# Optimization experiments

Measured on AMD Instinct MI355X. Metric: run time of the kernel, lower is better.

Reference implementation:

```python
import jax, jax.numpy as jnp
import numpy as np

B, C, H, W, NP = 4, 512, 32, 32, 2048
NH = 4
EPS = 1e-5


def setup_inputs() -> dict:
    key = jax.random.key(0)
    ks = jax.random.split(key, 12)
    s = 0.02
    d = {}
    d["img_feature"] = jax.random.normal(ks[0], (B, C, H, W), jnp.float32)
    d["point_feature"] = jax.random.normal(ks[1], (B, C, NP), jnp.float32)
    d["mlp_w1"] = jax.random.normal(ks[2], (2 * C, C), jnp.float32) * s
    d["mlp_b1"] = jnp.zeros((2 * C,), jnp.float32)
    d["bn1_gamma"] = jnp.ones((2 * C,), jnp.float32)
    d["bn1_beta"] = jnp.zeros((2 * C,), jnp.float32)
    d["bn1_mean"] = jnp.zeros((2 * C,), jnp.float32)
    d["bn1_var"] = jnp.ones((2 * C,), jnp.float32)
    d["mlp_w2"] = jax.random.normal(ks[3], (C, 2 * C), jnp.float32) * s
    d["mlp_b2"] = jnp.zeros((C,), jnp.float32)
    d["bn2_gamma"] = jnp.ones((C,), jnp.float32)
    d["bn2_beta"] = jnp.zeros((C,), jnp.float32)
    d["bn2_mean"] = jnp.zeros((C,), jnp.float32)
    d["bn2_var"] = jnp.ones((C,), jnp.float32)
    d["attn_qw"] = jax.random.normal(ks[4], (3, C, C), jnp.float32) * s
    d["attn_qb"] = jnp.zeros((3, C), jnp.float32)
    d["attn_kw"] = jax.random.normal(ks[5], (3, C, C), jnp.float32) * s
    d["attn_kb"] = jnp.zeros((3, C), jnp.float32)
    d["attn_vw"] = jax.random.normal(ks[6], (3, C, C), jnp.float32) * s
    d["attn_vb"] = jnp.zeros((3, C), jnp.float32)
    d["attn_ln_g"] = jnp.ones((3, C), jnp.float32)
    d["attn_ln_b"] = jnp.zeros((3, C), jnp.float32)
    return d


def _bn(x, g, b, m, v):  # x: [B, C, N], eval-mode batchnorm over channel dim
    return (x - m[:, None]) * jax.lax.rsqrt(v[:, None] + EPS) * g[:, None] + b[:, None]


def _mlp(x, w1, b1, g1, be1, m1, v1, w2, b2, g2, be2, m2, v2):
    # 1x1 Conv1d == per-position linear over channels
    y = jnp.einsum('oc,bcn->bon', w1, x) + b1[:, None]
    y = jax.nn.relu(_bn(y, g1, be1, m1, v1))
    z = jnp.einsum('oc,bcn->bon', w2, y) + b2[:, None]
    return jax.nn.relu(_bn(z, g2, be2, m2, v2))


def _self_attn(x, qw, qb, kw, kb, vw, vb, lng, lnb):
    # x: [B, S, E]; NOTE: original scales by 1/sqrt(hidden_size), not head_dim
    Bq, S, E = x.shape
    Hd = E // NH
    q = (jnp.einsum('bse,de->bsd', x, qw) + qb).reshape(Bq, S, NH, Hd)
    k = (jnp.einsum('bse,de->bsd', x, kw) + kb).reshape(Bq, S, NH, Hd)
    v = (jnp.einsum('bse,de->bsd', x, vw) + vb).reshape(Bq, S, NH, Hd)
    scores = jnp.einsum('bqhd,bkhd->bhqk', q, k) * (float(E) ** -0.5)
    attn = jax.nn.softmax(scores, axis=-1)
    out = jnp.einsum('bhqk,bkhd->bqhd', attn, v).reshape(Bq, S, E)
    y = out + x
    mu = jnp.mean(y, axis=-1, keepdims=True)
    var = jnp.var(y, axis=-1, keepdims=True)
    return (y - mu) * jax.lax.rsqrt(var + EPS) * lng + lnb


def reference(img_feature, point_feature, mlp_w1, mlp_b1, bn1_gamma, bn1_beta,
              bn1_mean, bn1_var, mlp_w2, mlp_b2, bn2_gamma, bn2_beta, bn2_mean,
              bn2_var, attn_qw, attn_qb, attn_kw, attn_kb, attn_vw, attn_vb,
              attn_ln_g, attn_ln_b):
    b, c, h, w = img_feature.shape
    i_in = img_feature.reshape(b, c, h * w)  # [B, C, N_i]
    mlp_args = (mlp_w1, mlp_b1, bn1_gamma, bn1_beta, bn1_mean, bn1_var,
                mlp_w2, mlp_b2, bn2_gamma, bn2_beta, bn2_mean, bn2_var)
    p_feat = _mlp(point_feature, *mlp_args)  # [B, C, N_p]
    i_feat = _mlp(i_in, *mlp_args)           # [B, C, N_i]
    phi = jnp.einsum('bcp,bci->bpi', p_feat, i_feat) * (float(c) ** -0.5)
    phi_p = jax.nn.softmax(phi, axis=1)   # softmax over points
    phi_i = jax.nn.softmax(phi, axis=-1)  # softmax over image positions
    I_enh = jnp.einsum('bcp,bpi->bci', p_feat, phi_p)  # [B, C, N_i]
    P_enh = jnp.einsum('bci,bpi->bcp', i_feat, phi_i)  # [B, C, N_p]
    att = lambda x, j: _self_attn(x, attn_qw[j], attn_qb[j], attn_kw[j],
                                  attn_kb[j], attn_vw[j], attn_vb[j],
                                  attn_ln_g[j], attn_ln_b[j])
    I = att(jnp.swapaxes(I_enh, 1, 2), 0)  # [B, N_i, C]
    P = att(jnp.swapaxes(P_enh, 1, 2), 1)  # [B, N_p, C]
    joint = jnp.concatenate([P, I], axis=1)  # [B, N_p + N_i, C]
    return att(joint, 2)
```

## Files before the change

kernel.cpp:

```cpp
#include <hip/hip_runtime.h>
#include <math.h>

#define LN_EPS 1e-5f

typedef __attribute__((ext_vector_type(8))) short bf16x8;
typedef __attribute__((ext_vector_type(4))) float f32x4;

#define GLDS16(g, l) __builtin_amdgcn_global_load_lds( \
    (const __attribute__((address_space(1))) unsigned int*)(g), \
    (__attribute__((address_space(3))) unsigned int*)(l), 16, 0, 0)

__device__ __forceinline__ float b2f(unsigned short h) { return __uint_as_float(((unsigned)h) << 16); }
__device__ __forceinline__ unsigned short f2b(float f) {
  unsigned u = __float_as_uint(f);
  unsigned r = (u + 0x7fffu + ((u >> 16) & 1u)) >> 16;
  return (unsigned short)r;
}
__device__ __forceinline__ float ld(const float* p) { return *p; }
__device__ __forceinline__ float ld(const unsigned short* p) { return b2f(*p); }
__device__ __forceinline__ void st(float* p, float v) { *p = v; }
__device__ __forceinline__ void st(unsigned short* p, float v) { *p = f2b(v); }

__device__ __forceinline__ float bred_sum(float v, float* red) {
  for (int o = 32; o; o >>= 1) v += __shfl_down(v, o, 64);
  int wid = threadIdx.x >> 6;
  __syncthreads();
  if ((threadIdx.x & 63) == 0) red[wid] = v;
  __syncthreads();
  return red[0] + red[1] + red[2] + red[3];
}

__global__ void prep_all(
    const float* __restrict__ w1, const float* __restrict__ w2, const float* __restrict__ vw,
    const float* __restrict__ qw, const float* __restrict__ qb,
    const float* __restrict__ kw, const float* __restrict__ kb,
    const float* __restrict__ b1, const float* __restrict__ g1, const float* __restrict__ be1,
    const float* __restrict__ m1, const float* __restrict__ v1,
    const float* __restrict__ b2, const float* __restrict__ g2, const float* __restrict__ be2,
    const float* __restrict__ m2, const float* __restrict__ v2,
    unsigned short* __restrict__ w1b, unsigned short* __restrict__ w2b,
    unsigned short* __restrict__ vwb, unsigned short* __restrict__ qkw,
    float* __restrict__ qkbias, float* __restrict__ s1, float* __restrict__ f1,
    float* __restrict__ s2, float* __restrict__ f2)
{
  const float scl = 0.044194173824159216f * 1.4426950408889634f;
  int idx = blockIdx.x * 256 + threadIdx.x;
  {
    int j = idx >> 19; int r = idx & 524287; int n = r >> 9; int k = r & 511;
    float v = (n < 512) ? qw[j * 262144 + n * 512 + k] * scl
                        : kw[j * 262144 + (n - 512) * 512 + k];
    qkw[idx] = f2b(v);
  }
  if (idx < 524288) { w1b[idx] = f2b(w1[idx]); w2b[idx] = f2b(w2[idx]); }
  if (idx < 786432) vwb[idx] = f2b(vw[idx]);
  if (idx < 3072) {
    int j = idx >> 10, n = idx & 1023;
    qkbias[idx] = (n < 512) ? qb[j * 512 + n] * scl : kb[j * 512 + n - 512];
  }
  if (idx < 1024) { float s = g1[idx] * rsqrtf(v1[idx] + LN_EPS); s1[idx] = s; f1[idx] = (b1[idx] - m1[idx]) * s + be1[idx]; }
  if (idx < 512)  { float s = g2[idx] * rsqrtf(v2[idx] + LN_EPS); s2[idx] = s; f2[idx] = (b2[idx] - m2[idx]) * s + be2[idx]; }
}

template<typename TS, typename TD>
__global__ __launch_bounds__(256) void transpose_t(const TS* __restrict__ src,
    TD* __restrict__ dst, int R, int Cc, long sS, long sD) {
  __shared__ float t[32][33];
  src += (long)blockIdx.z * sS; dst += (long)blockIdx.z * sD;
  int c0 = blockIdx.x * 32, r0 = blockIdx.y * 32;
  int tx = threadIdx.x & 31, ty = threadIdx.x >> 5;
#pragma unroll
  for (int rr = 0; rr < 32; rr += 8) t[ty + rr][tx] = ld(&src[(long)(r0 + ty + rr) * Cc + c0 + tx]);
  __syncthreads();
#pragma unroll
  for (int rr = 0; rr < 32; rr += 8) st(&dst[(long)(c0 + ty + rr) * R + r0 + tx], t[tx][ty + rr]);
}

template<int PER>
__global__ __launch_bounds__(256) void softmax_k(const float* __restrict__ x,
    unsigned short* __restrict__ y, long bstr) {
  __shared__ float red[4];
  const int L = PER * 256;
  int b = blockIdx.y, r = blockIdx.x, tid = threadIdx.x;
  const float* p = x + (long)b * bstr + (long)r * L;
  unsigned short* o = y + (long)b * bstr + (long)r * L;
  float vals[PER];
  float mx = -1e30f;
#pragma unroll
  for (int t = 0; t < PER; t++) { float v = p[tid + (t << 8)]; vals[t] = v; mx = fmaxf(mx, v); }
  for (int ofs = 32; ofs; ofs >>= 1) mx = fmaxf(mx, __shfl_down(mx, ofs, 64));
  int wid = tid >> 6;
  if ((tid & 63) == 0) red[wid] = mx;
  __syncthreads();
  mx = fmaxf(fmaxf(red[0], red[1]), fmaxf(red[2], red[3]));
  float sm = 0.f;
#pragma unroll
  for (int t = 0; t < PER; t++) { float e = __expf(vals[t] - mx); vals[t] = e; sm += e; }
  sm = bred_sum(sm, red);
  float inv = 1.f / sm;
#pragma unroll
  for (int t = 0; t < PER; t++) o[tid + (t << 8)] = f2b(vals[t] * inv);
}

template<int EPI, typename TC>
__global__ __launch_bounds__(256) void gemm_bf16(
    const unsigned short* __restrict__ A, long sA, int lda,
    const unsigned short* __restrict__ B, long sB, int ldb,
    TC* __restrict__ C, long sC, int ldc,
    int M, int N, int K,
    const float* __restrict__ sc, const float* __restrict__ bi, float cscale)
{
  __shared__ short As[128 * 64];
  __shared__ short Bs[128 * 64];
  const int tid = threadIdx.x;
  const int lane = tid & 63, wid = tid >> 6;
  const int wm = wid >> 1, wn = wid & 1;
  const int l15 = lane & 15, l4 = lane >> 4, l7 = lane & 7;
  const int bm = blockIdx.y * 128, bn = blockIdx.x * 128;
  const int srow = lane >> 3;
  A += (long)blockIdx.z * sA; B += (long)blockIdx.z * sB; C += (long)blockIdx.z * sC;
  float* CT = nullptr;
  if (EPI == 5) CT = (float*)bi + (long)blockIdx.z * sC;
  f32x4 acc[4][4] = {};
  for (int k0 = 0; k0 < K; k0 += 64) {
#pragma unroll
    for (int i = 0; i < 4; i++) {
      int row = (wid * 4 + i) * 8 + srow;
      int gcol = (l7 ^ (row & 7)) * 8;
      GLDS16(A + (long)(bm + row) * lda + k0 + gcol, &As[(wid * 4 + i) * 512]);
      GLDS16(B + (long)(bn + row) * ldb + k0 + gcol, &Bs[(wid * 4 + i) * 512]);
    }
    __syncthreads();
#pragma unroll
    for (int ks = 0; ks < 2; ks++) {
      bf16x8 af[4], bfr[4];
#pragma unroll
      for (int t = 0; t < 4; t++) {
        int ra = wm * 64 + t * 16 + l15;
        int rb = wn * 64 + t * 16 + l15;
        int ch = (l4 + 4 * ks) ^ (l15 & 7);
        af[t]  = *(const bf16x8*)&As[ra * 64 + ch * 8];
        bfr[t] = *(const bf16x8*)&Bs[rb * 64 + ch * 8];
      }
#pragma unroll
      for (int i = 0; i < 4; i++)
#pragma unroll
        for (int j2 = 0; j2 < 4; j2++)
          acc[i][j2] = __builtin_amdgcn_mfma_f32_16x16x32_bf16(af[i], bfr[j2], acc[i][j2], 0, 0, 0);
    }
    __syncthreads();
  }
#pragma unroll
  for (int i = 0; i < 4; i++) {
#pragma unroll
    for (int j2 = 0; j2 < 4; j2++) {
      int n = bn + wn * 64 + j2 * 16 + l15;
#pragma unroll
      for (int j = 0; j < 4; j++) {
        int m = bm + wm * 64 + i * 16 + l4 * 4 + j;
        float v = acc[i][j2][j];
        if (EPI == 1) v = fmaxf(fmaf(v, sc[n], bi[n]), 0.f);
        if (EPI == 2) v *= cscale;
        if (EPI == 3) v += bi[n];
        if (EPI == 4) v += bi[m];
        if (EPI == 5) { v *= cscale; CT[(long)n * M + m] = v; }
        st(&C[(long)m * ldc + n], v);
      }
    }
  }
}

__global__ __launch_bounds__(512) void attn_flash(
    const unsigned short* __restrict__ qk, const unsigned short* __restrict__ vT,
    unsigned short* __restrict__ out, int S)
{
  __shared__ short Ks[64 * 128];
  __shared__ short Vs[128 * 64];
  __shared__ short Ps[8][1024];
  const int tid = threadIdx.x, lane = tid & 63, wid = tid >> 6;
  const int h = blockIdx.y, b = blockIdx.z;
  const int l15 = lane & 15, l4 = lane >> 4, l7 = l15 & 7;
  const long qkb = (long)b * S * 1024;
  const long vbb = (long)b * 512 * S;
  const long obase = (long)b * S * 512;
  const int qr0 = blockIdx.x * 128 + wid * 16;
  const int kR0 = tid >> 4, kC0 = tid & 15;
  const int kR1 = (tid + 512) >> 4, kC1 = tid & 15;
  const int vR0 = tid >> 3, vC0 = tid & 7;
  const int vR1 = (tid + 512) >> 3, vC1 = tid & 7;
  bf16x8 qf[4];
#pragma unroll
  for (int ks = 0; ks < 4; ks++)
    qf[ks] = *(const bf16x8*)(qk + qkb + (long)(qr0 + l15) * 1024 + h * 128 + l4 * 8 + ks * 32);
  bf16x8 onev;
#pragma unroll
  for (int j = 0; j < 8; j++) onev[j] = (short)0x3F80;
  f32x4 O[8] = {};
  f32x4 Ol = {};
  float m_run = -1e30f;
  const int NT = S >> 6;
  int4 kr0, kr1, vr0, vr1;
  auto load_regs = [&](int kt) {
    kr0 = *(const int4*)(qk + qkb + (long)(kt * 64 + kR0) * 1024 + 512 + h * 128 + kC0 * 8);
    kr1 = *(const int4*)(qk + qkb + (long)(kt * 64 + kR1) * 1024 + 512 + h * 128 + kC1 * 8);
    vr0 = *(const int4*)(vT + vbb + (long)(h * 128 + vR0) * S + kt * 64 + vC0 * 8);
    vr1 = *(const int4*)(vT + vbb + (long)(h * 128 + vR1) * S + kt * 64 + vC1 * 8);
  };
  load_regs(0);
  for (int kt = 0; kt < NT; kt++) {
    __syncthreads();
    *(int4*)&Ks[kR0 * 128 + ((kC0 ^ (kR0 & 7)) << 3)] = kr0;
    *(int4*)&Ks[kR1 * 128 + ((kC1 ^ (kR1 & 7)) << 3)] = kr1;
    *(int4*)&Vs[vR0 * 64 + ((vC0 ^ (vR0 & 7)) << 3)] = vr0;
    *(int4*)&Vs[vR1 * 64 + ((vC1 ^ (vR1 & 7)) << 3)] = vr1;
    __syncthreads();
    if (kt + 1 < NT) load_regs(kt + 1);
    f32x4 sacc[4] = {};
    __builtin_amdgcn_s_setprio(1);
#pragma unroll
    for (int f = 0; f < 4; f++) {
      int row = f * 16 + l15;
#pragma unroll
      for (int ks = 0; ks < 4; ks++) {
        bf16x8 kf = *(const bf16x8*)&Ks[row * 128 + (((l4 + 4 * ks) ^ l7) << 3)];
        sacc[f] = __builtin_amdgcn_mfma_f32_16x16x32_bf16(kf, qf[ks], sacc[f], 0, 0, 0);
      }
    }
    __builtin_amdgcn_s_setprio(0);
    float pmax = fmaxf(fmaxf(sacc[0][0], sacc[0][1]), sacc[0][2]);
    pmax = fmaxf(fmaxf(pmax, sacc[0][3]), sacc[1][0]);
    pmax = fmaxf(fmaxf(pmax, sacc[1][1]), sacc[1][2]);
    pmax = fmaxf(fmaxf(pmax, sacc[1][3]), sacc[2][0]);
    pmax = fmaxf(fmaxf(pmax, sacc[2][1]), sacc[2][2]);
    pmax = fmaxf(fmaxf(pmax, sacc[2][3]), sacc[3][0]);
    pmax = fmaxf(fmaxf(pmax, sacc[3][1]), sacc[3][2]);
    pmax = fmaxf(pmax, sacc[3][3]);
    pmax = fmaxf(pmax, __shfl_xor(pmax, 16, 64));
    pmax = fmaxf(pmax, __shfl_xor(pmax, 32, 64));
    if (!__all(pmax - m_run <= 8.f)) {
      float m_new = fmaxf(m_run, pmax);
      float corr = __builtin_exp2f(m_run - m_new);
      m_run = m_new;
      Ol[0] *= corr; Ol[1] *= corr; Ol[2] *= corr; Ol[3] *= corr;
#pragma unroll
      for (int fd = 0; fd < 8; fd++) {
        O[fd][0] *= corr; O[fd][1] *= corr; O[fd][2] *= corr; O[fd][3] *= corr;
      }
    }
#pragma unroll
    for (int f = 0; f < 4; f++) {
      float e0 = __builtin_exp2f(sacc[f][0] - m_run);
      float e1 = __builtin_exp2f(sacc[f][1] - m_run);
      float e2 = __builtin_exp2f(sacc[f][2] - m_run);
      float e3 = __builtin_exp2f(sacc[f][3] - m_run);
      unsigned w0, w1;
      asm("v_cvt_pk_bf16_f32 %0, %1, %2" : "=v"(w0) : "v"(e0), "v"(e1));
      asm("v_cvt_pk_bf16_f32 %0, %1, %2" : "=v"(w1) : "v"(e2), "v"(e3));
      int2 pw; pw.x = (int)w0; pw.y = (int)w1;
      *(int2*)&Ps[wid][l15 * 64 + (((2 * f + (l4 >> 1)) ^ l7) << 3) + (l4 & 1) * 4] = pw;
    }
    __builtin_amdgcn_s_setprio(1);
#pragma unroll
    for (int ks = 0; ks < 2; ks++) {
      int pch = ((l4 + 4 * ks) ^ l7) << 3;
      bf16x8 pf = *(const bf16x8*)&Ps[wid][l15 * 64 + pch];
      Ol = __builtin_amdgcn_mfma_f32_16x16x32_bf16(onev, pf, Ol, 0, 0, 0);
#pragma unroll
      for (int fd = 0; fd < 8; fd++) {
        bf16x8 vf = *(const bf16x8*)&Vs[(fd * 16 + l15) * 64 + pch];
        O[fd] = __builtin_amdgcn_mfma_f32_16x16x32_bf16(vf, pf, O[fd], 0, 0, 0);
      }
    }
    __builtin_amdgcn_s_setprio(0);
  }
  float inv = 1.f / Ol[0];
  unsigned short* op = out + obase + (long)(qr0 + l15) * 512 + h * 128;
#pragma unroll
  for (int fd = 0; fd < 8; fd++) {
    ushort4 ov;
    ov.x = f2b(O[fd][0] * inv);
    ov.y = f2b(O[fd][1] * inv);
    ov.z = f2b(O[fd][2] * inv);
    ov.w = f2b(O[fd][3] * inv);
    *(ushort4*)&op[fd * 16 + l4 * 4] = ov;
  }
}

template<typename TD>
__global__ __launch_bounds__(256) void add_ln(
    const unsigned short* __restrict__ att, const unsigned short* __restrict__ resid,
    const float* __restrict__ g, const float* __restrict__ bt,
    TD* __restrict__ dst, long db, int S)
{
  __shared__ float red[4];
  int b = blockIdx.y, s = blockIdx.x, tid = threadIdx.x;
  const unsigned short* ap = att + ((long)b * S + s) * 512;
  const unsigned short* rp = resid + ((long)b * S + s) * 512;
  float y0 = b2f(ap[tid]) + b2f(rp[tid]);
  float y1 = b2f(ap[tid + 256]) + b2f(rp[tid + 256]);
  float mu = bred_sum(y0 + y1, red) * (1.f / 512.f);
  float d0 = y0 - mu, d1 = y1 - mu;
  float var = bred_sum(d0 * d0 + d1 * d1, red) * (1.f / 512.f);
  float rsv = rsqrtf(var + LN_EPS);
  TD* dp = dst + (long)b * db + (long)s * 512;
  st(&dp[tid], d0 * rsv * g[tid] + bt[tid]);
  st(&dp[tid + 256], d1 * rsv * g[tid + 256] + bt[tid + 256]);
}

extern "C" void kernel_launch(void* const* d_in, const int* in_sizes, int n_in,
                              void* d_out, int out_size, void* d_ws, size_t ws_size,
                              hipStream_t stream) {
  (void)in_sizes; (void)n_in; (void)out_size; (void)ws_size;
  const float* img = (const float*)d_in[0];
  const float* pts = (const float*)d_in[1];
  const float* w1  = (const float*)d_in[2];
  const float* b1  = (const float*)d_in[3];
  const float* g1  = (const float*)d_in[4];
  const float* be1 = (const float*)d_in[5];
  const float* m1  = (const float*)d_in[6];
  const float* v1  = (const float*)d_in[7];
  const float* w2  = (const float*)d_in[8];
  const float* b2  = (const float*)d_in[9];
  const float* g2  = (const float*)d_in[10];
  const float* be2 = (const float*)d_in[11];
  const float* m2  = (const float*)d_in[12];
  const float* v2  = (const float*)d_in[13];
  const float* qw  = (const float*)d_in[14];
  const float* qb  = (const float*)d_in[15];
  const float* kw  = (const float*)d_in[16];
  const float* kb  = (const float*)d_in[17];
  const float* vw  = (const float*)d_in[18];
  const float* vb  = (const float*)d_in[19];
  const float* lng = (const float*)d_in[20];
  const float* lnb = (const float*)d_in[21];
  float* out = (float*)d_out;
  float* ws  = (float*)d_ws;
  typedef unsigned short u16;

  u16*   xTu   = (u16*)ws;
  float* phi   = ws;
  u16*   y1u   = (u16*)(ws + 8388608);
  float* phiT  = ws + 8388608;
  u16*   featu = (u16*)(ws + 16777216);
  u16*   featTu= (u16*)(ws + 19922944);
  u16*   smI   = (u16*)(ws + 23068672);
  u16*   smPT  = (u16*)(ws + 27262976);
  u16*   Xi    = (u16*)(ws + 31457280);
  u16*   Xp    = (u16*)(ws + 32505856);
  u16*   jointu= (u16*)(ws + 34603008);
  u16*   w1b   = (u16*)(ws + 37748736);
  u16*   w2b   = (u16*)(ws + 38010880);
  u16*   qkwb  = (u16*)(ws + 38273024);
  u16*   vwb   = (u16*)(ws + 39059456);
  float* s1f   = ws + 39452672;
  float* f1f   = s1f + 1024;
  float* s2f   = f1f + 1024;
  float* f2f   = s2f + 512;
  float* qkbf  = ws + 39455744;
  u16*   qkbu  = (u16*)ws;
  u16*   vTu   = (u16*)(ws + 6291456);
  u16*   attu  = (u16*)(ws + 9437184);

  dim3 blk(256);
  prep_all<<<dim3(6144), blk, 0, stream>>>(w1, w2, vw, qw, qb, kw, kb,
      b1, g1, be1, m1, v1, b2, g2, be2, m2, v2,
      w1b, w2b, vwb, qkwb, qkbf, s1f, f1f, s2f, f2f);

  transpose_t<float, u16><<<dim3(64, 16, 4), blk, 0, stream>>>(pts, xTu, 512, 2048, 1048576L, 1572864L);
  transpose_t<float, u16><<<dim3(32, 16, 4), blk, 0, stream>>>(img, xTu + 1048576, 512, 1024, 524288L, 1572864L);

  gemm_bf16<1, u16><<<dim3(8, 24, 4), blk, 0, stream>>>(xTu, 1572864L, 512, w1b, 0L, 512,
      y1u, 3145728L, 1024, 3072, 1024, 512, s1f, f1f, 0.f);
  gemm_bf16<1, u16><<<dim3(4, 24, 4), blk, 0, stream>>>(y1u, 3145728L, 1024, w2b, 0L, 1024,
      featu, 1572864L, 512, 3072, 512, 1024, s2f, f2f, 0.f);
  transpose_t<u16, u16><<<dim3(16, 96, 4), blk, 0, stream>>>(featu, featTu, 3072, 512, 1572864L, 1572864L);
  gemm_bf16<5, float><<<dim3(8, 16, 4), blk, 0, stream>>>(featu, 1572864L, 512, featu + 1048576, 1572864L, 512,
      phi, 2097152L, 1024, 2048, 1024, 512, nullptr, (const float*)phiT, 0.044194173824159216f);
  softmax_k<4><<<dim3(2048, 4), blk, 0, stream>>>(phi, smI, 2097152L);
  softmax_k<8><<<dim3(1024, 4), blk, 0, stream>>>(phiT, smPT, 2097152L);
  gemm_bf16<0, u16><<<dim3(4, 8, 4), blk, 0, stream>>>(smPT, 2097152L, 2048, featTu, 1572864L, 3072,
      Xi, 524288L, 512, 1024, 512, 2048, nullptr, nullptr, 0.f);
  gemm_bf16<0, u16><<<dim3(4, 16, 4), blk, 0, stream>>>(smI, 2097152L, 1024, featTu + 2048, 1572864L, 3072,
      Xp, 1048576L, 512, 2048, 512, 1024, nullptr, nullptr, 0.f);

  struct AttCfg { const u16* X; int S; int j; };
  AttCfg cfgs[3] = { {Xi, 1024, 0}, {Xp, 2048, 1}, {jointu, 3072, 2} };
  for (int a = 0; a < 3; a++) {
    const u16* X = cfgs[a].X; int S = cfgs[a].S; int j = cfgs[a].j;
    long xs = (long)S * 512;
    gemm_bf16<3, u16><<<dim3(8, S / 128, 4), blk, 0, stream>>>(X, xs, 512, qkwb + j * 524288, 0L, 512,
        qkbu, (long)S * 1024, 1024, S, 1024, 512, nullptr, qkbf + j * 1024, 0.f);
    gemm_bf16<4, u16><<<dim3(S / 128, 4, 4), blk, 0, stream>>>(vwb + j * 262144, 0L, 512, X, xs, 512,
        vTu, xs, S, 512, S, 512, nullptr, vb + j * 512, 0.f);
    attn_flash<<<dim3(S / 128, 4, 4), dim3(512), 0, stream>>>(qkbu, vTu, attu, S);
    if (a == 0)
      add_ln<u16><<<dim3(S, 4), blk, 0, stream>>>(attu, X, lng + j * 512, lnb + j * 512,
          jointu + 1048576, 1572864L, S);
    else if (a == 1)
      add_ln<u16><<<dim3(S, 4), blk, 0, stream>>>(attu, X, lng + j * 512, lnb + j * 512,
          jointu, 1572864L, S);
    else
      add_ln<float><<<dim3(S, 4), blk, 0, stream>>>(attu, X, lng + j * 512, lnb + j * 512,
          out, 1572864L, S);
  }
}
```

Before: 521.2 us.

## Batch independent image and point attention branches into paired launches, fuse feature transpose

```diff
diff --git a/kernel.cpp b/kernel.cpp
--- a/kernel.cpp
+++ b/kernel.cpp
@@ -5,6 +5,7 @@
 
 typedef __attribute__((ext_vector_type(8))) short bf16x8;
 typedef __attribute__((ext_vector_type(4))) float f32x4;
+typedef unsigned short u16t;
 
 #define GLDS16(g, l) __builtin_amdgcn_global_load_lds( \
     (const __attribute__((address_space(1))) unsigned int*)(g), \
@@ -101,25 +102,28 @@
   for (int t = 0; t < PER; t++) o[tid + (t << 8)] = f2b(vals[t] * inv);
 }
 
+template<typename TC>
+struct GArgs {
+  const unsigned short* A; long sA; int lda;
+  const unsigned short* B; long sB; int ldb;
+  TC* C; long sC; int ldc;
+  int M, N, K;
+  const float* sc; const float* bi; float cscale; TC* ct;
+};
+
 template<int EPI, typename TC>
-__global__ __launch_bounds__(256) void gemm_bf16(
-    const unsigned short* __restrict__ A, long sA, int lda,
-    const unsigned short* __restrict__ B, long sB, int ldb,
-    TC* __restrict__ C, long sC, int ldc,
-    int M, int N, int K,
-    const float* __restrict__ sc, const float* __restrict__ bi, float cscale)
-{
-  __shared__ short As[128 * 64];
-  __shared__ short Bs[128 * 64];
+__device__ __forceinline__ void gemm_body(short* As, short* Bs,
+    const unsigned short* __restrict__ A, int lda,
+    const unsigned short* __restrict__ B, int ldb,
+    TC* __restrict__ C, int ldc, int M, int K,
+    const float* sc, const float* bi, float cscale, TC* ct,
+    int bm, int bn)
+{
   const int tid = threadIdx.x;
   const int lane = tid & 63, wid = tid >> 6;
   const int wm = wid >> 1, wn = wid & 1;
   const int l15 = lane & 15, l4 = lane >> 4, l7 = lane & 7;
-  const int bm = blockIdx.y * 128, bn = blockIdx.x * 128;
   const int srow = lane >> 3;
-  A += (long)blockIdx.z * sA; B += (long)blockIdx.z * sB; C += (long)blockIdx.z * sC;
-  float* CT = nullptr;
-  if (EPI == 5) CT = (float*)bi + (long)blockIdx.z * sC;
   f32x4 acc[4][4] = {};
   for (int k0 = 0; k0 < K; k0 += 64) {
 #pragma unroll
@@ -158,31 +162,50 @@
       for (int j = 0; j < 4; j++) {
         int m = bm + wm * 64 + i * 16 + l4 * 4 + j;
         float v = acc[i][j2][j];
-        if (EPI == 1) v = fmaxf(fmaf(v, sc[n], bi[n]), 0.f);
+        if (EPI == 1 || EPI == 6) v = fmaxf(fmaf(v, sc[n], bi[n]), 0.f);
         if (EPI == 2) v *= cscale;
         if (EPI == 3) v += bi[n];
         if (EPI == 4) v += bi[m];
-        if (EPI == 5) { v *= cscale; CT[(long)n * M + m] = v; }
+        if (EPI == 5) v *= cscale;
+        if (EPI == 5 || EPI == 6) st(&ct[(long)n * M + m], v);
         st(&C[(long)m * ldc + n], v);
       }
     }
   }
 }
 
-__global__ __launch_bounds__(512) void attn_flash(
+template<int EPI, typename TC>
+__global__ __launch_bounds__(256) void gemm_bf16(GArgs<TC> g) {
+  __shared__ short As[128 * 64];
+  __shared__ short Bs[128 * 64];
+  int b = blockIdx.z;
+  gemm_body<EPI, TC>(As, Bs, g.A + (long)b * g.sA, g.lda, g.B + (long)b * g.sB, g.ldb,
+      g.C + (long)b * g.sC, g.ldc, g.M, g.K, g.sc, g.bi, g.cscale,
+      g.ct ? g.ct + (long)b * g.sC : (TC*)nullptr, blockIdx.y * 128, blockIdx.x * 128);
+}
+
+template<int EPI, typename TC>
+__global__ __launch_bounds__(256) void gemm_pair(GArgs<TC> g0, GArgs<TC> g1, int mb0, int nb0) {
+  __shared__ short As[128 * 64];
+  __shared__ short Bs[128 * 64];
+  int cfg = blockIdx.z >> 2, b = blockIdx.z & 3;
+  if (!cfg && ((int)blockIdx.y >= mb0 || (int)blockIdx.x >= nb0)) return;
+  const GArgs<TC>& g = cfg ? g1 : g0;
+  gemm_body<EPI, TC>(As, Bs, g.A + (long)b * g.sA, g.lda, g.B + (long)b * g.sB, g.ldb,
+      g.C + (long)b * g.sC, g.ldc, g.M, g.K, g.sc, g.bi, g.cscale,
+      g.ct ? g.ct + (long)b * g.sC : (TC*)nullptr, blockIdx.y * 128, blockIdx.x * 128);
+}
+
+__device__ __forceinline__ void attn_body(short* Ks, short* Vs, short* Ps,
     const unsigned short* __restrict__ qk, const unsigned short* __restrict__ vT,
-    unsigned short* __restrict__ out, int S)
-{
-  __shared__ short Ks[64 * 128];
-  __shared__ short Vs[128 * 64];
-  __shared__ short Ps[8][1024];
+    unsigned short* __restrict__ out, int S, int qblk, int h, int b)
+{
   const int tid = threadIdx.x, lane = tid & 63, wid = tid >> 6;
-  const int h = blockIdx.y, b = blockIdx.z;
   const int l15 = lane & 15, l4 = lane >> 4, l7 = l15 & 7;
   const long qkb = (long)b * S * 1024;
   const long vbb = (long)b * 512 * S;
   const long obase = (long)b * S * 512;
-  const int qr0 = blockIdx.x * 128 + wid * 16;
+  const int qr0 = qblk * 128 + wid * 16;
   const int kR0 = tid >> 4, kC0 = tid & 15;
   const int kR1 = (tid + 512) >> 4, kC1 = tid & 15;
   const int vR0 = tid >> 3, vC0 = tid & 7;
@@ -256,13 +279,13 @@
       asm("v_cvt_pk_bf16_f32 %0, %1, %2" : "=v"(w0) : "v"(e0), "v"(e1));
       asm("v_cvt_pk_bf16_f32 %0, %1, %2" : "=v"(w1) : "v"(e2), "v"(e3));
       int2 pw; pw.x = (int)w0; pw.y = (int)w1;
-      *(int2*)&Ps[wid][l15 * 64 + (((2 * f + (l4 >> 1)) ^ l7) << 3) + (l4 & 1) * 4] = pw;
+      *(int2*)&Ps[wid * 1024 + l15 * 64 + (((2 * f + (l4 >> 1)) ^ l7) << 3) + (l4 & 1) * 4] = pw;
     }
     __builtin_amdgcn_s_setprio(1);
 #pragma unroll
     for (int ks = 0; ks < 2; ks++) {
       int pch = ((l4 + 4 * ks) ^ l7) << 3;
-      bf16x8 pf = *(const bf16x8*)&Ps[wid][l15 * 64 + pch];
+      bf16x8 pf = *(const bf16x8*)&Ps[wid * 1024 + l15 * 64 + pch];
       Ol = __builtin_amdgcn_mfma_f32_16x16x32_bf16(onev, pf, Ol, 0, 0, 0);
 #pragma unroll
       for (int fd = 0; fd < 8; fd++) {
@@ -276,34 +299,90 @@
   unsigned short* op = out + obase + (long)(qr0 + l15) * 512 + h * 128;
 #pragma unroll
   for (int fd = 0; fd < 8; fd++) {
-    ushort4 ov;
-    ov.x = f2b(O[fd][0] * inv);
-    ov.y = f2b(O[fd][1] * inv);
-    ov.z = f2b(O[fd][2] * inv);
-    ov.w = f2b(O[fd][3] * inv);
-    *(ushort4*)&op[fd * 16 + l4 * 4] = ov;
-  }
+    float a0 = O[fd][0] * inv, a1 = O[fd][1] * inv;
+    float a2 = O[fd][2] * inv, a3 = O[fd][3] * inv;
+    unsigned wA, wB;
+    asm("v_cvt_pk_bf16_f32 %0, %1, %2" : "=v"(wA) : "v"(a0), "v"(a1));
+    asm("v_cvt_pk_bf16_f32 %0, %1, %2" : "=v"(wB) : "v"(a2), "v"(a3));
+    int2 ov; ov.x = (int)wA; ov.y = (int)wB;
+    *(int2*)&op[fd * 16 + l4 * 4] = ov;
+  }
+}
+
+__global__ __launch_bounds__(512) void attn_flash(
+    const unsigned short* __restrict__ qk, const unsigned short* __restrict__ vT,
+    unsigned short* __restrict__ out, int S)
+{
+  __shared__ short Ks[64 * 128];
+  __shared__ short Vs[128 * 64];
+  __shared__ short Ps[8 * 1024];
+  attn_body(Ks, Vs, Ps, qk, vT, out, S, blockIdx.x, blockIdx.y, blockIdx.z);
+}
+
+__global__ __launch_bounds__(512) void attn_flash_pair(
+    const unsigned short* __restrict__ qk0, const unsigned short* __restrict__ vT0,
+    unsigned short* __restrict__ out0, int S0,
+    const unsigned short* __restrict__ qk1, const unsigned short* __restrict__ vT1,
+    unsigned short* __restrict__ out1, int S1)
+{
+  __shared__ short Ks[64 * 128];
+  __shared__ short Vs[128 * 64];
+  __shared__ short Ps[8 * 1024];
+  int cfg = blockIdx.z >> 2, b = blockIdx.z & 3;
+  const unsigned short* qk = cfg ? qk1 : qk0;
+  const unsigned short* vT = cfg ? vT1 : vT0;
+  unsigned short* out = cfg ? out1 : out0;
+  int S = cfg ? S1 : S0;
+  if ((int)blockIdx.x * 128 >= S) return;
+  attn_body(Ks, Vs, Ps, qk, vT, out, S, blockIdx.x, blockIdx.y, b);
 }
 
 template<typename TD>
-__global__ __launch_bounds__(256) void add_ln(
-    const unsigned short* __restrict__ att, const unsigned short* __restrict__ resid,
-    const float* __restrict__ g, const float* __restrict__ bt,
-    TD* __restrict__ dst, long db, int S)
-{
-  __shared__ float red[4];
-  int b = blockIdx.y, s = blockIdx.x, tid = threadIdx.x;
-  const unsigned short* ap = att + ((long)b * S + s) * 512;
-  const unsigned short* rp = resid + ((long)b * S + s) * 512;
+__device__ __forceinline__ void add_ln_body(
+    const unsigned short* ap, const unsigned short* rp,
+    const float* g, const float* bt, TD* dp, float* red)
+{
+  int tid = threadIdx.x;
   float y0 = b2f(ap[tid]) + b2f(rp[tid]);
   float y1 = b2f(ap[tid + 256]) + b2f(rp[tid + 256]);
   float mu = bred_sum(y0 + y1, red) * (1.f / 512.f);
   float d0 = y0 - mu, d1 = y1 - mu;
   float var = bred_sum(d0 * d0 + d1 * d1, red) * (1.f / 512.f);
   float rsv = rsqrtf(var + LN_EPS);
-  TD* dp = dst + (long)b * db + (long)s * 512;
   st(&dp[tid], d0 * rsv * g[tid] + bt[tid]);
   st(&dp[tid + 256], d1 * rsv * g[tid + 256] + bt[tid + 256]);
+}
+
+template<typename TD>
+__global__ __launch_bounds__(256) void add_ln(
+    const unsigned short* __restrict__ att, const unsigned short* __restrict__ resid,
+    const float* __restrict__ g, const float* __restrict__ bt,
+    TD* __restrict__ dst, long db, int S)
+{
+  __shared__ float red[4];
+  int b = blockIdx.y, s = blockIdx.x;
+  add_ln_body<TD>(att + ((long)b * S + s) * 512, resid + ((long)b * S + s) * 512,
+                  g, bt, dst + (long)b * db + (long)s * 512, red);
+}
+
+__global__ __launch_bounds__(256) void add_ln_pair(
+    const unsigned short* __restrict__ att0, const unsigned short* __restrict__ res0,
+    const float* __restrict__ g0, const float* __restrict__ bt0,
+    unsigned short* __restrict__ dst0, long db0, int S0,
+    const unsigned short* __restrict__ att1, const unsigned short* __restrict__ res1,
+    const float* __restrict__ g1, const float* __restrict__ bt1,
+    unsigned short* __restrict__ dst1, long db1, int S1)
+{
+  __shared__ float red[4];
+  int b = blockIdx.y, s = blockIdx.x, cfg = blockIdx.z;
+  if (cfg == 0) {
+    if (s >= S0) return;
+    add_ln_body<unsigned short>(att0 + ((long)b * S0 + s) * 512, res0 + ((long)b * S0 + s) * 512,
+                                g0, bt0, dst0 + (long)b * db0 + (long)s * 512, red);
+  } else {
+    add_ln_body<unsigned short>(att1 + ((long)b * S1 + s) * 512, res1 + ((long)b * S1 + s) * 512,
+                                g1, bt1, dst1 + (long)b * db1 + (long)s * 512, red);
+  }
 }
 
 extern "C" void kernel_launch(void* const* d_in, const int* in_sizes, int n_in,
@@ -356,9 +435,15 @@
   float* s2f   = f1f + 1024;
   float* f2f   = s2f + 512;
   float* qkbf  = ws + 39455744;
+  u16*   qk0   = (u16*)ws;
+  u16*   qk1   = (u16*)(ws + 2097152);
+  u16*   vT0   = (u16*)(ws + 6291456);
+  u16*   vT1   = (u16*)(ws + 7340032);
+  u16*   out0  = (u16*)(ws + 9437184);
+  u16*   out1  = (u16*)(ws + 10485760);
   u16*   qkbu  = (u16*)ws;
   u16*   vTu   = (u16*)(ws + 6291456);
-  u16*   attu  = (u16*)(ws + 9437184);
+  u16*   attu2 = (u16*)(ws + 9437184);
 
   dim3 blk(256);
   prep_all<<<dim3(6144), blk, 0, stream>>>(w1, w2, vw, qw, qb, kw, kb,
@@ -368,38 +453,44 @@
   transpose_t<float, u16><<<dim3(64, 16, 4), blk, 0, stream>>>(pts, xTu, 512, 2048, 1048576L, 1572864L);
   transpose_t<float, u16><<<dim3(32, 16, 4), blk, 0, stream>>>(img, xTu + 1048576, 512, 1024, 524288L, 1572864L);
 
-  gemm_bf16<1, u16><<<dim3(8, 24, 4), blk, 0, stream>>>(xTu, 1572864L, 512, w1b, 0L, 512,
-      y1u, 3145728L, 1024, 3072, 1024, 512, s1f, f1f, 0.f);
-  gemm_bf16<1, u16><<<dim3(4, 24, 4), blk, 0, stream>>>(y1u, 3145728L, 1024, w2b, 0L, 1024,
-      featu, 1572864L, 512, 3072, 512, 1024, s2f, f2f, 0.f);
-  transpose_t<u16, u16><<<dim3(16, 96, 4), blk, 0, stream>>>(featu, featTu, 3072, 512, 1572864L, 1572864L);
-  gemm_bf16<5, float><<<dim3(8, 16, 4), blk, 0, stream>>>(featu, 1572864L, 512, featu + 1048576, 1572864L, 512,
-      phi, 2097152L, 1024, 2048, 1024, 512, nullptr, (const float*)phiT, 0.044194173824159216f);
+  gemm_bf16<1, u16><<<dim3(8, 24, 4), blk, 0, stream>>>(
+      GArgs<u16>{xTu, 1572864L, 512, w1b, 0L, 512, y1u, 3145728L, 1024,
+                 3072, 1024, 512, s1f, f1f, 0.f, nullptr});
+  gemm_bf16<6, u16><<<dim3(4, 24, 4), blk, 0, stream>>>(
+      GArgs<u16>{y1u, 3145728L, 1024, w2b, 0L, 1024, featu, 1572864L, 512,
+                 3072, 512, 1024, s2f, f2f, 0.f, featTu});
+  gemm_bf16<5, float><<<dim3(8, 16, 4), blk, 0, stream>>>(
+      GArgs<float>{featu, 1572864L, 512, featu + 1048576, 1572864L, 512, phi, 2097152L, 1024,
+                   2048, 1024, 512, nullptr, nullptr, 0.044194173824159216f, phiT});
   softmax_k<4><<<dim3(2048, 4), blk, 0, stream>>>(phi, smI, 2097152L);
   softmax_k<8><<<dim3(1024, 4), blk, 0, stream>>>(phiT, smPT, 2097152L);
-  gemm_bf16<0, u16><<<dim3(4, 8, 4), blk, 0, stream>>>(smPT, 2097152L, 2048, featTu, 1572864L, 3072,
-      Xi, 524288L, 512, 1024, 512, 2048, nullptr, nullptr, 0.f);
-  gemm_bf16<0, u16><<<dim3(4, 16, 4), blk, 0, stream>>>(smI, 2097152L, 1024, featTu + 2048, 1572864L, 3072,
-      Xp, 1048576L, 512, 2048, 512, 1024, nullptr, nullptr, 0.f);
-
-  struct AttCfg { const u16* X; int S; int j; };
-  AttCfg cfgs[3] = { {Xi, 1024, 0}, {Xp, 2048, 1}, {jointu, 3072, 2} };
-  for (int a = 0; a < 3; a++) {
-    const u16* X = cfgs[a].X; int S = cfgs[a].S; int j = cfgs[a].j;
-    long xs = (long)S * 512;
-    gemm_bf16<3, u16><<<dim3(8, S / 128, 4), blk, 0, stream>>>(X, xs, 512, qkwb + j * 524288, 0L, 512,
-        qkbu, (long)S * 1024, 1024, S, 1024, 512, nullptr, qkbf + j * 1024, 0.f);
-    gemm_bf16<4, u16><<<dim3(S / 128, 4, 4), blk, 0, stream>>>(vwb + j * 262144, 0L, 512, X, xs, 512,
-        vTu, xs, S, 512, S, 512, nullptr, vb + j * 512, 0.f);
-    attn_flash<<<dim3(S / 128, 4, 4), dim3(512), 0, stream>>>(qkbu, vTu, attu, S);
-    if (a == 0)
-      add_ln<u16><<<dim3(S, 4), blk, 0, stream>>>(attu, X, lng + j * 512, lnb + j * 512,
-          jointu + 1048576, 1572864L, S);
-    else if (a == 1)
-      add_ln<u16><<<dim3(S, 4), blk, 0, stream>>>(attu, X, lng + j * 512, lnb + j * 512,
-          jointu, 1572864L, S);
-    else
-      add_ln<float><<<dim3(S, 4), blk, 0, stream>>>(attu, X, lng + j * 512, lnb + j * 512,
-          out, 1572864L, S);
-  }
-}
+  gemm_pair<0, u16><<<dim3(4, 16, 8), blk, 0, stream>>>(
+      GArgs<u16>{smPT, 2097152L, 2048, featTu, 1572864L, 3072, Xi, 524288L, 512,
+                 1024, 512, 2048, nullptr, nullptr, 0.f, nullptr},
+      GArgs<u16>{smI, 2097152L, 1024, featTu + 2048, 1572864L, 3072, Xp, 1048576L, 512,
+                 2048, 512, 1024, nullptr, nullptr, 0.f, nullptr}, 8, 4);
+  gemm_pair<3, u16><<<dim3(8, 16, 8), blk, 0, stream>>>(
+      GArgs<u16>{Xi, 524288L, 512, qkwb, 0L, 512, qk0, 1048576L, 1024,
+                 1024, 1024, 512, nullptr, qkbf, 0.f, nullptr},
+      GArgs<u16>{Xp, 1048576L, 512, qkwb + 524288, 0L, 512, qk1, 2097152L, 1024,
+                 2048, 1024, 512, nullptr, qkbf + 1024, 0.f, nullptr}, 8, 8);
+  gemm_pair<4, u16><<<dim3(16, 4, 8), blk, 0, stream>>>(
+      GArgs<u16>{vwb, 0L, 512, Xi, 524288L, 512, vT0, 524288L, 1024,
+                 512, 1024, 512, nullptr, vb, 0.f, nullptr},
+      GArgs<u16>{vwb + 262144, 0L, 512, Xp, 1048576L, 512, vT1, 1048576L, 2048,
+                 512, 2048, 512, nullptr, vb + 512, 0.f, nullptr}, 4, 8);
+  attn_flash_pair<<<dim3(16, 4, 8), dim3(512), 0, stream>>>(
+      qk0, vT0, out0, 1024, qk1, vT1, out1, 2048);
+  add_ln_pair<<<dim3(2048, 4, 2), blk, 0, stream>>>(
+      out0, Xi, lng, lnb, jointu + 1048576, 1572864L, 1024,
+      out1, Xp, lng + 512, lnb + 512, jointu, 1572864L, 2048);
+  gemm_bf16<3, u16><<<dim3(8, 24, 4), blk, 0, stream>>>(
+      GArgs<u16>{jointu, 1572864L, 512, qkwb + 1048576, 0L, 512, qkbu, 3145728L, 1024,
+                 3072, 1024, 512, nullptr, qkbf + 2048, 0.f, nullptr});
+  gemm_bf16<4, u16><<<dim3(24, 4, 4), blk, 0, stream>>>(
+      GArgs<u16>{vwb + 524288, 0L, 512, jointu, 1572864L, 512, vTu, 1572864L, 3072,
+                 512, 3072, 512, nullptr, vb + 1024, 0.f, nullptr});
+  attn_flash<<<dim3(24, 4, 4), dim3(512), 0, stream>>>(qkbu, vTu, attu2, 3072);
+  add_ln<float><<<dim3(3072, 4), blk, 0, stream>>>(attu2, jointu,
+      lng + 1024, lnb + 1024, out, 1572864L, 3072);
+}
```

Result: faster. 465.3 us (-10.7%).
